# Performance work log

Measured on AMD Instinct MI355X. Metric: run time of the kernel, lower is better.

## Reference

```python
import jax, jax.numpy as jnp
import numpy as np

HIDDEN = 2048
N_HEADS = 32
N_KV = 8
HEAD_DIM = 128
EPS = 1e-6
THETA = 10000.0
WINDOW = 512
T = 2048


def _rms_norm(x, w, eps=EPS):
    # x: [..., d]
    var = jnp.mean(x * x, axis=-1, keepdims=True)
    return x * jax.lax.rsqrt(var + eps) * w


def _rope(x, positions):
    # neox-style full rotary, x: [T, H, d]
    d = x.shape[-1]
    inv_freq = 1.0 / (THETA ** (jnp.arange(0, d, 2, dtype=jnp.float32) / d))  # [d/2]
    ang = positions.astype(jnp.float32)[:, None] * inv_freq  # [T, d/2]
    cos = jnp.cos(ang)[:, None, :]  # [T,1,d/2]
    sin = jnp.sin(ang)[:, None, :]
    x1, x2 = x[..., : d // 2], x[..., d // 2 :]
    return jnp.concatenate([x1 * cos - x2 * sin, x2 * cos + x1 * sin], axis=-1)


def setup_inputs() -> dict:
    key = jax.random.key(0)
    ks = jax.random.split(key, 6)
    q_size = N_HEADS * HEAD_DIM
    kv_size = N_KV * HEAD_DIM
    s = 1.0 / np.sqrt(HIDDEN)
    return {
        "positions": jnp.arange(T, dtype=jnp.int32),
        "hidden_states": jax.random.normal(ks[0], (T, HIDDEN), dtype=jnp.float32),
        "w_qkv": jax.random.normal(ks[1], (HIDDEN, q_size + 2 * kv_size), dtype=jnp.float32) * s,
        "w_o": jax.random.normal(ks[2], (q_size, HIDDEN), dtype=jnp.float32) * s,
        "w_g": jax.random.normal(ks[3], (HIDDEN, N_HEADS), dtype=jnp.float32) * s,
        "q_norm_w": jnp.ones((HEAD_DIM,), dtype=jnp.float32),
        "k_norm_w": jnp.ones((HEAD_DIM,), dtype=jnp.float32),
    }


def reference(positions, hidden_states, w_qkv, w_o, w_g, q_norm_w, k_norm_w):
    t = hidden_states.shape[0]
    q_size = N_HEADS * HEAD_DIM
    kv_size = N_KV * HEAD_DIM
    scale = HEAD_DIM ** -0.5
    group = N_HEADS // N_KV

    qkv = hidden_states @ w_qkv  # [T, q+2kv]
    q = qkv[:, :q_size].reshape(t, N_HEADS, HEAD_DIM)
    k = qkv[:, q_size : q_size + kv_size].reshape(t, N_KV, HEAD_DIM)
    v = qkv[:, q_size + kv_size :].reshape(t, N_KV, HEAD_DIM)

    # per-head RMSNorm then RoPE
    q = _rope(_rms_norm(q, q_norm_w), positions)
    k = _rope(_rms_norm(k, k_norm_w), positions)

    # sliding-window causal attention with GQA (group queries per kv head)
    qg = q.reshape(t, N_KV, group, HEAD_DIM)
    scores = jnp.einsum("tkgd,skd->kgts", qg, k) * scale  # [Hkv,G,T,T]
    diff = positions[:, None] - positions[None, :]  # i - j
    mask = (diff >= 0) & (diff < WINDOW)  # causal + sliding window
    scores = jnp.where(mask[None, None], scores, -jnp.inf)
    probs = jax.nn.softmax(scores, axis=-1)
    attn = jnp.einsum("kgts,skd->tkgd", probs, v).reshape(t, N_HEADS, HEAD_DIM)

    # softplus gate per head, then output projection
    gate = jax.nn.softplus((hidden_states @ w_g).astype(jnp.float32)).astype(attn.dtype)
    attn = attn * gate[:, :, None]
    return attn.reshape(t, q_size) @ w_o
```

## Files before the change

### kernel.cpp

```cpp
#include <hip/hip_runtime.h>

typedef __attribute__((ext_vector_type(4))) float floatx4;
typedef __attribute__((ext_vector_type(8))) _Float16 half8;
typedef __attribute__((ext_vector_type(4))) _Float16 half4;

#define TT 2048
#define HIDDEN 2048
#define NH 32
#define NKV 8
#define HD 128
#define QSIZE 4096
#define KVSIZE 1024
#define QKVN 6144
#define QKVNP 6272
#define WQR 6400
#define VOFF 5120
#define GOFF 6144
#define WINDOW 512

__global__ __launch_bounds__(256) void prep_kernel(
    const float* __restrict__ w_qkv, const float* __restrict__ w_o,
    const float* __restrict__ hidden, const float* __restrict__ w_g,
    _Float16* __restrict__ Wqkvt, _Float16* __restrict__ Wot,
    _Float16* __restrict__ Xb) {
  __shared__ float tile[64][68];
  int bid = blockIdx.x;
  int tid = threadIdx.x;
  if (bid >= 5120) {
    if (bid < 7168) {
      int i = ((bid - 5120) * 256 + tid) * 8;
      float4 a = *(const float4*)&hidden[i];
      float4 b = *(const float4*)&hidden[i + 4];
      alignas(16) _Float16 o[8] = {(_Float16)a.x, (_Float16)a.y, (_Float16)a.z, (_Float16)a.w,
                                   (_Float16)b.x, (_Float16)b.y, (_Float16)b.z, (_Float16)b.w};
      *(uint4*)&Xb[i] = *(const uint4*)o;
    } else if (bid < 7392) {
      int i = ((bid - 7168) * 256 + tid) * 8;
      *(uint4*)&Wqkvt[(size_t)(GOFF + NH) * HIDDEN + i] = (uint4){0, 0, 0, 0};
    } else {
      int br = (bid - 7392) * 32;
      int c = tid & 31, r0 = tid >> 5;
      __shared__ float gt[32][33];
#pragma unroll
      for (int i = 0; i < 4; ++i) {
        int r = r0 + 8 * i;
        gt[r][c] = w_g[(size_t)(br + r) * NH + c];
      }
      __syncthreads();
#pragma unroll
      for (int i = 0; i < 4; ++i) {
        int r = r0 + 8 * i;
        Wqkvt[(size_t)(GOFF + r) * HIDDEN + br + c] = (_Float16)gt[c][r];
      }
    }
    return;
  }
  const float* in;
  _Float16* out;
  int R, C, tilesX, t;
  if (bid < 3072) { in = w_qkv; out = Wqkvt; R = HIDDEN; C = QKVN; tilesX = 96; t = bid; }
  else           { in = w_o;   out = Wot;   R = QSIZE;  C = HIDDEN; tilesX = 32; t = bid - 3072; }
  int bc = (t % tilesX) * 64, br = (t / tilesX) * 64;
  int rr = tid >> 4, l16 = tid & 15;
#pragma unroll
  for (int it = 0; it < 4; ++it) {
    int r = rr + it * 16;
    *(float4*)&tile[r][l16 * 4] = *(const float4*)&in[(size_t)(br + r) * C + bc + l16 * 4];
  }
  __syncthreads();
  int orow = tid >> 2, rr0 = (tid & 3) * 16;
  alignas(16) _Float16 tmp[16];
#pragma unroll
  for (int jj = 0; jj < 16; ++jj) tmp[jj] = (_Float16)tile[rr0 + jj][orow];
  *(uint4*)&out[(size_t)(bc + orow) * R + br + rr0] = *(const uint4*)&tmp[0];
  *(uint4*)&out[(size_t)(bc + orow) * R + br + rr0 + 8] = *(const uint4*)&tmp[8];
}

__global__ __launch_bounds__(256) void repack_v_kernel(const _Float16* __restrict__ QKVh,
                                                       _Float16* __restrict__ Vf) {
  __shared__ _Float16 tile[64][136];
  int st = blockIdx.x, kh = blockIdx.y;
  int s0 = st * 64;
#pragma unroll
  for (int i = 0; i < 4; ++i) {
    int c = threadIdx.x + i * 256;
    int row = c >> 4, part = c & 15;
    *(uint4*)&tile[row][part * 8] =
        *(const uint4*)&QKVh[(size_t)(s0 + row) * QKVNP + VOFF + kh * HD + part * 8];
  }
  __syncthreads();
  _Float16* dst = Vf + (size_t)(kh * 32 + st) * 8192;
#pragma unroll
  for (int i = 0; i < 4; ++i) {
    int c = threadIdx.x + i * 256;
    int jd = c >> 7, kc = (c >> 6) & 1, quad = (c >> 4) & 3, n16 = c & 15;
    int d = jd * 16 + n16, sb = kc * 32 + quad * 8;
    alignas(16) _Float16 tmp[8];
#pragma unroll
    for (int j = 0; j < 8; ++j) tmp[j] = tile[sb + j][d];
    *(uint4*)&dst[c * 8] = *(const uint4*)tmp;
  }
}

__device__ __forceinline__ void async16(const _Float16* g, _Float16* l) {
  __builtin_amdgcn_global_load_lds((const __attribute__((address_space(1))) void*)g,
                                   (__attribute__((address_space(3))) void*)l, 16, 0, 0);
}

#define G256_K 2048

#define STG_A(ob, mh, kt)                                                        \
  async16(As0 + (size_t)(mh) * 64 * G256_K + (kt), &lds[(ob) + ((mh) * 64 + r0A0) * 64]); \
  async16(As1 + (size_t)(mh) * 64 * G256_K + (kt), &lds[(ob) + ((mh) * 64 + r0A1) * 64]);
#define STG_B(ob, nh, kt)                                                        \
  async16(Bs0 + (size_t)(nh) * 32 * G256_K + (kt), &lds[(ob) + 16384 + ((nh) * 32 + r0B0) * 64]); \
  async16(Bs1 + (size_t)(nh) * 32 * G256_K + (kt), &lds[(ob) + 16384 + ((nh) * 32 + r0B1) * 64]);

#define LD_A(DST, mh)                                                            \
  _Pragma("unroll") for (int fm = 0; fm < 4; ++fm)                               \
  _Pragma("unroll") for (int ks = 0; ks < 2; ++ks)                               \
    DST[fm][ks] = *(const half8*)&LA[(wm * 128 + (mh) * 64 + fm * 16 + lr) * 64 + \
                                     (((ks * 4 + quad) ^ l7) * 8)];
#define LD_B(DST, nh)                                                            \
  _Pragma("unroll") for (int fn = 0; fn < 2; ++fn)                               \
  _Pragma("unroll") for (int ks = 0; ks < 2; ++ks)                               \
    DST[fn][ks] = *(const half8*)&LB[(wn * 64 + (nh) * 32 + fn * 16 + lr) * 64 + \
                                     (((ks * 4 + quad) ^ l7) * 8)];
#define MFMAQ(AS, BS, mh, nh)                                                    \
  __builtin_amdgcn_s_setprio(1);                                                 \
  _Pragma("unroll") for (int fm = 0; fm < 4; ++fm)                               \
  _Pragma("unroll") for (int fn = 0; fn < 2; ++fn)                               \
  _Pragma("unroll") for (int ks = 0; ks < 2; ++ks)                               \
    acc[(mh) * 4 + fm][(nh) * 2 + fn] = __builtin_amdgcn_mfma_f32_16x16x32_f16(  \
        AS[fm][ks], BS[fn][ks], acc[(mh) * 4 + fm][(nh) * 2 + fn], 0, 0, 0);     \
  __builtin_amdgcn_s_setprio(0);
#define VMW0 asm volatile("s_waitcnt vmcnt(0)" ::: "memory")
#define BAR __builtin_amdgcn_s_barrier()
#define SB0 __builtin_amdgcn_sched_barrier(0)

__global__ __launch_bounds__(512, 2) void gemm256_kernel(
    const _Float16* __restrict__ A, const _Float16* __restrict__ Bt,
    _Float16* __restrict__ C) {
  __shared__ _Float16 lds[65536];
  int tid = threadIdx.x;
  int wave = tid >> 6, lane = tid & 63;
  int wm = wave >> 2, wn = wave & 3;
  int lr = lane & 15, quad = lane >> 4, l7 = lane & 7, l3 = lane >> 3;
  int m0 = blockIdx.x * 256, n0 = blockIdx.y * 256;

  int q0 = wave * 2, q1 = q0 + 1;
  int r0A0 = (q0 >> 3) * 128 + (q0 & 7) * 8;
  int r0A1 = (q1 >> 3) * 128 + (q1 & 7) * 8;
  int r0B0 = (q0 >> 2) * 64 + (q0 & 3) * 8;
  int r0B1 = (q1 >> 2) * 64 + (q1 & 3) * 8;
  int gA8 = (l7 ^ l3) * 8;

  const _Float16* As0 = A + (size_t)(m0 + r0A0 + l3) * G256_K + gA8;
  const _Float16* As1 = A + (size_t)(m0 + r0A1 + l3) * G256_K + gA8;
  const _Float16* Bs0 = Bt + (size_t)(n0 + r0B0 + l3) * G256_K + gA8;
  const _Float16* Bs1 = Bt + (size_t)(n0 + r0B1 + l3) * G256_K + gA8;

  floatx4 acc[8][4];
#pragma unroll
  for (int i = 0; i < 8; ++i)
#pragma unroll
    for (int j = 0; j < 4; ++j) acc[i][j] = (floatx4){0.f, 0.f, 0.f, 0.f};

  STG_A(0, 0, 0);
  STG_A(0, 1, 0);
  STG_B(0, 0, 0);
  STG_B(0, 1, 0);
  VMW0;
  BAR;
  SB0;

  half8 a0f[4][2], a1f[4][2], b0[2][2], b1[2][2];

  for (int t = 0; t < 32; ++t) {
    int bb = (t & 1) << 15;
    int ob = bb ^ 32768;
    int ktn = (t + 1) * 64;
    bool stg = (t < 31);
    const _Float16* LA = &lds[bb];
    const _Float16* LB = &lds[bb + 16384];

    if (stg) {
      STG_A(ob, 0, ktn);
      STG_B(ob, 0, ktn);
      STG_B(ob, 1, ktn);
      STG_A(ob, 1, ktn);
    }

    LD_B(b0, 0);
    LD_A(a0f, 0);
    MFMAQ(a0f, b0, 0, 0);
    LD_B(b1, 1);
    MFMAQ(a0f, b1, 0, 1);
    LD_A(a1f, 1);
    MFMAQ(a1f, b0, 1, 0);
    MFMAQ(a1f, b1, 1, 1);

    if (stg) VMW0;
    BAR;
    SB0;
  }

#pragma unroll
  for (int mh = 0; mh < 2; ++mh)
#pragma unroll
    for (int fm = 0; fm < 4; ++fm)
#pragma unroll
      for (int nh = 0; nh < 2; ++nh)
#pragma unroll
        for (int fn = 0; fn < 2; ++fn)
#pragma unroll
          for (int rr = 0; rr < 4; ++rr) {
            int row = m0 + wm * 128 + mh * 64 + fm * 16 + quad * 4 + rr;
            int col = n0 + wn * 64 + nh * 32 + fn * 16 + lr;
            if (col < QKVNP)
              C[(size_t)row * QKVNP + col] = (_Float16)acc[mh * 4 + fm][nh * 2 + fn][rr];
          }
}

__device__ __forceinline__ void swizzle_mn(int& m0, int& n0) {
  int ntiles = gridDim.y;
  int pid = blockIdx.x + blockIdx.y * gridDim.x;
  int band = pid / (8 * ntiles);
  int wi = pid - band * (8 * ntiles);
  m0 = (band * 8 + (wi & 7)) * 128;
  n0 = (wi >> 3) * 128;
}

__global__ __launch_bounds__(256, 2) void gemm_bt_splitk_kernel(
    const _Float16* __restrict__ A, const _Float16* __restrict__ Bt,
    float* __restrict__ Cp, int M, int N, int K, int Ks) {
  __shared__ _Float16 As[128 * 64];
  __shared__ _Float16 Bs[128 * 64];
  int tid = threadIdx.x;
  int wave = tid >> 6, lane = tid & 63;
  int wm = wave >> 1, wn = wave & 1;
  int m0, n0;
  swizzle_mn(m0, n0);
  int kb = blockIdx.z * Ks;
  float* C = Cp + (size_t)blockIdx.z * M * N;
  int lr = lane & 15;
  int quad = lane >> 4;
  floatx4 acc[4][4];
#pragma unroll
  for (int i = 0; i < 4; ++i)
#pragma unroll
    for (int j = 0; j < 4; ++j) acc[i][j] = (floatx4){0.f, 0.f, 0.f, 0.f};

  for (int k0 = kb; k0 < kb + Ks; k0 += 64) {
    __syncthreads();
#pragma unroll
    for (int it = 0; it < 4; ++it) {
      int c = tid + it * 256;
      int row = c >> 3, j = c & 7;
      int jj = j ^ (row & 7);
      _Float16* la = &As[it * 2048 + wave * 512];
      _Float16* lb = &Bs[it * 2048 + wave * 512];
      async16(&A[(size_t)(m0 + row) * K + k0 + jj * 8], la);
      async16(&Bt[(size_t)(n0 + row) * K + k0 + jj * 8], lb);
    }
    __syncthreads();
#pragma unroll
    for (int kc = 0; kc < 2; ++kc) {
      int ch = kc * 4 + quad;
      half8 a[4], b[4];
#pragma unroll
      for (int i = 0; i < 4; ++i) {
        int r = wm * 64 + i * 16 + lr;
        a[i] = *(const half8*)&As[r * 64 + (ch ^ (r & 7)) * 8];
      }
#pragma unroll
      for (int j = 0; j < 4; ++j) {
        int r = wn * 64 + j * 16 + lr;
        b[j] = *(const half8*)&Bs[r * 64 + (ch ^ (r & 7)) * 8];
      }
#pragma unroll
      for (int i = 0; i < 4; ++i)
#pragma unroll
        for (int j = 0; j < 4; ++j)
          acc[i][j] = __builtin_amdgcn_mfma_f32_16x16x32_f16(a[i], b[j], acc[i][j], 0, 0, 0);
    }
  }
  int rq = quad * 4;
#pragma unroll
  for (int i = 0; i < 4; ++i)
#pragma unroll
    for (int j = 0; j < 4; ++j)
#pragma unroll
      for (int r = 0; r < 4; ++r) {
        int row = m0 + wm * 64 + i * 16 + rq + r;
        int col = n0 + wn * 64 + j * 16 + lr;
        C[(size_t)row * N + col] = acc[i][j][r];
      }
}

__global__ __launch_bounds__(256) void reduce2_kernel(const float* __restrict__ P,
                                                      float* __restrict__ out) {
  size_t i = ((size_t)blockIdx.x * 256 + threadIdx.x) * 8;
  const float* Q = P + (size_t)TT * HIDDEN;
  float4 a0 = *(const float4*)&P[i];
  float4 a1 = *(const float4*)&P[i + 4];
  float4 b0 = *(const float4*)&Q[i];
  float4 b1 = *(const float4*)&Q[i + 4];
  a0.x += b0.x; a0.y += b0.y; a0.z += b0.z; a0.w += b0.w;
  a1.x += b1.x; a1.y += b1.y; a1.z += b1.z; a1.w += b1.w;
  *(float4*)&out[i] = a0;
  *(float4*)&out[i + 4] = a1;
}

__global__ __launch_bounds__(256) void normrope_kernel(
    const _Float16* __restrict__ qkv, const float* __restrict__ qw,
    const float* __restrict__ kw, const int* __restrict__ positions,
    _Float16* __restrict__ qh, _Float16* __restrict__ Kf) {
  int wid = blockIdx.x * 4 + (threadIdx.x >> 6);
  int lane = threadIdx.x & 63;
  int t, hh;
  const _Float16* src;
  const float* w;
  bool isq = wid < TT * NH;
  if (isq) {
    t = wid >> 5; hh = wid & 31;
    src = qkv + (size_t)t * QKVNP + hh * HD;
    w = qw;
  } else {
    int r = wid - TT * NH;
    t = r >> 3; hh = r & 7;
    src = qkv + (size_t)t * QKVNP + QSIZE + hh * HD;
    w = kw;
  }
  float x1 = (float)src[lane];
  float x2 = (float)src[lane + 64];
  float ss = x1 * x1 + x2 * x2;
#pragma unroll
  for (int off = 1; off < 64; off <<= 1) ss += __shfl_xor(ss, off);
  float rr = rsqrtf(ss * (1.0f / 128.0f) + 1e-6f);
  float n1 = x1 * rr * w[lane];
  float n2 = x2 * rr * w[lane + 64];
  float pos = (float)positions[t];
  float invf = exp2f(-(float)lane * (13.287712379549449f / 64.0f));
  float ang = pos * invf;
  float sn, cs;
  sincosf(ang, &sn, &cs);
  float r1 = n1 * cs - n2 * sn;
  float r2 = n2 * cs + n1 * sn;
  if (isq) {
    _Float16* dst = qh + ((size_t)t * NH + hh) * HD;
    dst[lane] = (_Float16)r1;
    dst[lane + 64] = (_Float16)r2;
  } else {
    int st = t >> 6, jt = (t >> 4) & 3, n16 = t & 15;
    _Float16* kb = Kf + (size_t)(hh * 32 + st) * 8192;
    int c = jt * 256 + (lane >> 5) * 64 + ((lane >> 3) & 3) * 16 + n16;
    kb[c * 8 + (lane & 7)] = (_Float16)r1;
    kb[(c + 128) * 8 + (lane & 7)] = (_Float16)r2;
  }
}

#define PSTR 68
#define M0 8.0f
__global__ __launch_bounds__(256, 2) void attn_kernel(
    const _Float16* __restrict__ Qh, const _Float16* __restrict__ Kf,
    const _Float16* __restrict__ Vf, const _Float16* __restrict__ QKVh,
    _Float16* __restrict__ Og) {
  const float scale = 0.08838834764831845f;
  __shared__ _Float16 Ps[4][16 * PSTR];
  int tid = threadIdx.x;
  int wave = tid >> 6, lane = tid & 63;
  int n16 = lane & 15, quad = lane >> 4;
  int t0 = blockIdx.x * 16;
  int kh = blockIdx.y;
  int h = kh * 4 + wave;
  _Float16* ps = Ps[wave];

  half8 qf[4];
#pragma unroll
  for (int kc = 0; kc < 4; ++kc)
    qf[kc] = *(const half8*)&Qh[((size_t)(t0 + n16) * NH + h) * HD + kc * 32 + quad * 8];

  floatx4 O[8];
  float lp[4];
#pragma unroll
  for (int jd = 0; jd < 8; ++jd) O[jd] = (floatx4){0.f, 0.f, 0.f, 0.f};
#pragma unroll
  for (int r = 0; r < 4; ++r) lp[r] = 0.f;

  int lo = t0 - (WINDOW - 1);
  if (lo < 0) lo = 0;
  int st0 = lo >> 6;
  int st1 = t0 >> 6;

  half8 kfr[4][4];
  {
    const _Float16* kb = Kf + (size_t)(kh * 32 + st0) * 8192;
#pragma unroll
    for (int jt = 0; jt < 4; ++jt)
#pragma unroll
      for (int kc = 0; kc < 4; ++kc)
        kfr[jt][kc] = *(const half8*)&kb[(jt * 4 + kc) * 512 + lane * 8];
  }

  for (int st = st0; st <= st1; ++st) {
    int s0 = st * 64;
    const _Float16* vb = Vf + (size_t)(kh * 32 + st) * 8192;
    floatx4 S[4];
#pragma unroll
    for (int jt = 0; jt < 4; ++jt) S[jt] = (floatx4){0.f, 0.f, 0.f, 0.f};
#pragma unroll
    for (int jt = 0; jt < 4; ++jt)
#pragma unroll
      for (int kc = 0; kc < 4; ++kc)
        S[jt] = __builtin_amdgcn_mfma_f32_16x16x32_f16(qf[kc], kfr[jt][kc], S[jt], 0, 0, 0);
    if (st < st1) {
      const _Float16* kb = Kf + (size_t)(kh * 32 + st + 1) * 8192;
#pragma unroll
      for (int jt = 0; jt < 4; ++jt)
#pragma unroll
        for (int kc = 0; kc < 4; ++kc)
          kfr[jt][kc] = *(const half8*)&kb[(jt * 4 + kc) * 512 + lane * 8];
    }
    bool interior = (t0 >= s0 + 63) && (t0 + 15 - s0 < WINDOW);
    if (interior) {
#pragma unroll
      for (int r = 0; r < 4; ++r) {
        float rs = 0.f;
#pragma unroll
        for (int jt = 0; jt < 4; ++jt) {
          float p = __expf(__builtin_fmaf(S[jt][r], scale, -M0));
          rs += p;
          ps[(quad * 4 + r) * PSTR + jt * 16 + n16] = (_Float16)p;
        }
        lp[r] += rs;
      }
    } else {
#pragma unroll
      for (int r = 0; r < 4; ++r) {
        int tq = t0 + quad * 4 + r;
        float rs = 0.f;
#pragma unroll
        for (int jt = 0; jt < 4; ++jt) {
          int diff = tq - (s0 + jt * 16 + n16);
          bool ok = (diff >= 0) && (diff < WINDOW);
          float p = ok ? __expf(__builtin_fmaf(S[jt][r], scale, -M0)) : 0.f;
          rs += p;
          ps[(quad * 4 + r) * PSTR + jt * 16 + n16] = (_Float16)p;
        }
        lp[r] += rs;
      }
    }
    half8 pf[2];
#pragma unroll
    for (int kc = 0; kc < 2; ++kc) {
      half4 lo4 = *(const half4*)&ps[n16 * PSTR + kc * 32 + quad * 8];
      half4 hi4 = *(const half4*)&ps[n16 * PSTR + kc * 32 + quad * 8 + 4];
      pf[kc] = (half8){lo4[0], lo4[1], lo4[2], lo4[3], hi4[0], hi4[1], hi4[2], hi4[3]};
    }
#pragma unroll
    for (int jd = 0; jd < 8; ++jd) {
#pragma unroll
      for (int kc = 0; kc < 2; ++kc) {
        half8 vfr = *(const half8*)&vb[(jd * 2 + kc) * 512 + lane * 8];
        O[jd] = __builtin_amdgcn_mfma_f32_16x16x32_f16(pf[kc], vfr, O[jd], 0, 0, 0);
      }
    }
  }
#pragma unroll
  for (int r = 0; r < 4; ++r) {
    float l = lp[r];
#pragma unroll
    for (int off = 1; off < 16; off <<= 1) l += __shfl_xor(l, off);
    int t = t0 + quad * 4 + r;
    float gl = (float)QKVh[(size_t)t * QKVNP + GOFF + h];
    float g = (gl > 0.f) ? gl + log1pf(__expf(-gl)) : log1pf(__expf(gl));
    float inv = g / l;
#pragma unroll
    for (int jd = 0; jd < 8; ++jd)
      Og[(size_t)t * QSIZE + h * HD + jd * 16 + n16] = (_Float16)(O[jd][r] * inv);
  }
}

extern "C" void kernel_launch(void* const* d_in, const int* in_sizes, int n_in,
                              void* d_out, int out_size, void* d_ws, size_t ws_size,
                              hipStream_t stream) {
  const int* positions = (const int*)d_in[0];
  const float* hidden = (const float*)d_in[1];
  const float* w_qkv = (const float*)d_in[2];
  const float* w_o = (const float*)d_in[3];
  const float* w_g = (const float*)d_in[4];
  const float* q_norm_w = (const float*)d_in[5];
  const float* k_norm_w = (const float*)d_in[6];
  float* out = (float*)d_out;

  char* ws = (char*)d_ws;
  size_t off = 0;
  auto alloc = [&](size_t bytes) {
    void* p = ws + off;
    off += (bytes + 255) & ~(size_t)255;
    return p;
  };
  _Float16* Xb = (_Float16*)alloc((size_t)TT * HIDDEN * 2);
  _Float16* Wqkvt = (_Float16*)alloc((size_t)WQR * HIDDEN * 2);
  _Float16* Wot = (_Float16*)alloc((size_t)HIDDEN * QSIZE * 2);
  _Float16* QKVh = (_Float16*)alloc((size_t)TT * QKVNP * 2);
  _Float16* Qh = (_Float16*)alloc((size_t)TT * NH * HD * 2);
  _Float16* Kf = (_Float16*)alloc((size_t)NKV * 32 * 8192 * 2);
  _Float16* Vf = (_Float16*)alloc((size_t)NKV * 32 * 8192 * 2);
  _Float16* Og = (_Float16*)alloc((size_t)TT * QSIZE * 2);
  float* Cp = (float*)ws;

  prep_kernel<<<7456, 256, 0, stream>>>(w_qkv, w_o, hidden, w_g, Wqkvt, Wot, Xb);
  gemm256_kernel<<<dim3(TT / 256, WQR / 256), 512, 0, stream>>>(Xb, Wqkvt, QKVh);
  normrope_kernel<<<(TT * (NH + NKV)) / 4, 256, 0, stream>>>(QKVh, q_norm_w, k_norm_w,
                                                             positions, Qh, Kf);
  repack_v_kernel<<<dim3(32, NKV), 256, 0, stream>>>(QKVh, Vf);
  attn_kernel<<<dim3(TT / 16, NKV), 256, 0, stream>>>(Qh, Kf, Vf, QKVh, Og);
  gemm_bt_splitk_kernel<<<dim3(TT / 128, HIDDEN / 128, 2), 256, 0, stream>>>(
      Og, Wot, Cp, TT, HIDDEN, QSIZE, QSIZE / 2);
  reduce2_kernel<<<(TT * HIDDEN) / (256 * 8), 256, 0, stream>>>(Cp, out);
}
```

Before: 314.7 us.

## Fuse RMSNorm, RoPE, K/V repacking and gate extraction into the QKV GEMM epilogue

Each QKV GEMM tile epilogue now applies per-head RMSNorm and RoPE and writes Q and K directly in the layouts attention expects. It also scatters V into the attention-ready packed layout and writes the gate logits to a compact buffer. The prep kernel gains a precomputed cos/sin table. This removes the QKVh intermediate and the separate normrope and repack_v kernels, saving global round trips and launches. The cost is a heavier epilogue with LDS exchanges between paired waves, extra barriers and scattered 2-byte stores.

```diff
diff --git a/kernel.cpp b/kernel.cpp
--- a/kernel.cpp
+++ b/kernel.cpp
@@ -12,17 +12,16 @@
 #define QSIZE 4096
 #define KVSIZE 1024
 #define QKVN 6144
-#define QKVNP 6272
 #define WQR 6400
-#define VOFF 5120
 #define GOFF 6144
 #define WINDOW 512
 
 __global__ __launch_bounds__(256) void prep_kernel(
     const float* __restrict__ w_qkv, const float* __restrict__ w_o,
     const float* __restrict__ hidden, const float* __restrict__ w_g,
+    const int* __restrict__ positions,
     _Float16* __restrict__ Wqkvt, _Float16* __restrict__ Wot,
-    _Float16* __restrict__ Xb) {
+    _Float16* __restrict__ Xb, float* __restrict__ tbl) {
   __shared__ float tile[64][68];
   int bid = blockIdx.x;
   int tid = threadIdx.x;
@@ -37,7 +36,7 @@
     } else if (bid < 7392) {
       int i = ((bid - 7168) * 256 + tid) * 8;
       *(uint4*)&Wqkvt[(size_t)(GOFF + NH) * HIDDEN + i] = (uint4){0, 0, 0, 0};
-    } else {
+    } else if (bid < 7456) {
       int br = (bid - 7392) * 32;
       int c = tid & 31, r0 = tid >> 5;
       __shared__ float gt[32][33];
@@ -52,6 +51,15 @@
         int r = r0 + 8 * i;
         Wqkvt[(size_t)(GOFF + r) * HIDDEN + br + c] = (_Float16)gt[c][r];
       }
+    } else {
+      int idx = (bid - 7456) * 256 + tid;
+      int t = idx >> 6, j = idx & 63;
+      float pos = (float)positions[t];
+      float invf = exp2f(-(float)j * (13.287712379549449f / 64.0f));
+      float sn, cs;
+      sincosf(pos * invf, &sn, &cs);
+      tbl[t * 128 + j] = cs;
+      tbl[t * 128 + 64 + j] = sn;
     }
     return;
   }
@@ -74,32 +82,6 @@
   for (int jj = 0; jj < 16; ++jj) tmp[jj] = (_Float16)tile[rr0 + jj][orow];
   *(uint4*)&out[(size_t)(bc + orow) * R + br + rr0] = *(const uint4*)&tmp[0];
   *(uint4*)&out[(size_t)(bc + orow) * R + br + rr0 + 8] = *(const uint4*)&tmp[8];
-}
-
-__global__ __launch_bounds__(256) void repack_v_kernel(const _Float16* __restrict__ QKVh,
-                                                       _Float16* __restrict__ Vf) {
-  __shared__ _Float16 tile[64][136];
-  int st = blockIdx.x, kh = blockIdx.y;
-  int s0 = st * 64;
-#pragma unroll
-  for (int i = 0; i < 4; ++i) {
-    int c = threadIdx.x + i * 256;
-    int row = c >> 4, part = c & 15;
-    *(uint4*)&tile[row][part * 8] =
-        *(const uint4*)&QKVh[(size_t)(s0 + row) * QKVNP + VOFF + kh * HD + part * 8];
-  }
-  __syncthreads();
-  _Float16* dst = Vf + (size_t)(kh * 32 + st) * 8192;
-#pragma unroll
-  for (int i = 0; i < 4; ++i) {
-    int c = threadIdx.x + i * 256;
-    int jd = c >> 7, kc = (c >> 6) & 1, quad = (c >> 4) & 3, n16 = c & 15;
-    int d = jd * 16 + n16, sb = kc * 32 + quad * 8;
-    alignas(16) _Float16 tmp[8];
-#pragma unroll
-    for (int j = 0; j < 8; ++j) tmp[j] = tile[sb + j][d];
-    *(uint4*)&dst[c * 8] = *(const uint4*)tmp;
-  }
 }
 
 __device__ __forceinline__ void async16(const _Float16* g, _Float16* l) {
@@ -140,7 +122,10 @@
 
 __global__ __launch_bounds__(512, 2) void gemm256_kernel(
     const _Float16* __restrict__ A, const _Float16* __restrict__ Bt,
-    _Float16* __restrict__ C) {
+    const float* __restrict__ tbl, const float* __restrict__ qw,
+    const float* __restrict__ kw, _Float16* __restrict__ Qh,
+    _Float16* __restrict__ Kf, _Float16* __restrict__ Vf,
+    _Float16* __restrict__ Gate) {
   __shared__ _Float16 lds[65536];
   int tid = threadIdx.x;
   int wave = tid >> 6, lane = tid & 63;
@@ -205,21 +190,137 @@
     SB0;
   }
 
-#pragma unroll
-  for (int mh = 0; mh < 2; ++mh)
-#pragma unroll
-    for (int fm = 0; fm < 4; ++fm)
-#pragma unroll
-      for (int nh = 0; nh < 2; ++nh)
-#pragma unroll
-        for (int fn = 0; fn < 2; ++fn)
-#pragma unroll
-          for (int rr = 0; rr < 4; ++rr) {
-            int row = m0 + wm * 128 + mh * 64 + fm * 16 + quad * 4 + rr;
-            int col = n0 + wn * 64 + nh * 32 + fn * 16 + lr;
-            if (col < QKVNP)
-              C[(size_t)row * QKVNP + col] = (_Float16)acc[mh * 4 + fm][nh * 2 + fn][rr];
-          }
+  int nt = blockIdx.y;
+  int wn1 = wn & 1;
+  int hloc = wn >> 1;
+
+  if (nt < 20) {
+    const float* w = (nt < 16) ? qw : kw;
+    float wlo[2][2], whi[2][2];
+#pragma unroll
+    for (int nh = 0; nh < 2; ++nh)
+#pragma unroll
+      for (int fn = 0; fn < 2; ++fn) {
+        int c0 = nh * 32 + fn * 16 + lr;
+        wlo[nh][fn] = w[c0];
+        whi[nh][fn] = w[c0 + 64];
+      }
+    _Float16* ldh = lds;
+    float* lsum = (float*)&lds[8 * 64 * 68];
+#pragma unroll
+    for (int mh = 0; mh < 2; ++mh) {
+      float s[4][4];
+#pragma unroll
+      for (int fm = 0; fm < 4; ++fm)
+#pragma unroll
+        for (int rq = 0; rq < 4; ++rq) {
+          float sv = 0.f;
+#pragma unroll
+          for (int nh = 0; nh < 2; ++nh)
+#pragma unroll
+            for (int fn = 0; fn < 2; ++fn) {
+              float v = acc[mh * 4 + fm][nh * 2 + fn][rq];
+              sv += v * v;
+            }
+#pragma unroll
+          for (int off = 1; off < 16; off <<= 1) sv += __shfl_xor(sv, off);
+          s[fm][rq] = sv;
+        }
+#pragma unroll
+      for (int fm = 0; fm < 4; ++fm)
+#pragma unroll
+        for (int nh = 0; nh < 2; ++nh)
+#pragma unroll
+          for (int fn = 0; fn < 2; ++fn)
+#pragma unroll
+            for (int rq = 0; rq < 4; ++rq) {
+              int row = fm * 16 + quad * 4 + rq;
+              ldh[(wave * 64 + row) * 68 + nh * 32 + fn * 16 + lr] =
+                  (_Float16)acc[mh * 4 + fm][nh * 2 + fn][rq];
+            }
+      if (lr == 0) {
+#pragma unroll
+        for (int fm = 0; fm < 4; ++fm)
+#pragma unroll
+          for (int rq = 0; rq < 4; ++rq)
+            lsum[wave * 64 + fm * 16 + quad * 4 + rq] = s[fm][rq];
+      }
+      __syncthreads();
+      int pw = wave ^ 1;
+#pragma unroll
+      for (int fm = 0; fm < 4; ++fm)
+#pragma unroll
+        for (int rq = 0; rq < 4; ++rq) {
+          int row = fm * 16 + quad * 4 + rq;
+          int t = m0 + wm * 128 + mh * 64 + row;
+          float inv = rsqrtf((s[fm][rq] + lsum[pw * 64 + row]) * 0.0078125f + 1e-6f);
+          const float* tb = &tbl[(size_t)t * 128];
+#pragma unroll
+          for (int nh = 0; nh < 2; ++nh)
+#pragma unroll
+            for (int fn = 0; fn < 2; ++fn) {
+              int c0 = nh * 32 + fn * 16 + lr;
+              float xo = acc[mh * 4 + fm][nh * 2 + fn][rq];
+              float xp = (float)ldh[(pw * 64 + row) * 68 + c0];
+              float cs = tb[c0], sn = tb[64 + c0];
+              float out;
+              if (wn1 == 0)
+                out = (xo * inv * wlo[nh][fn]) * cs - (xp * inv * whi[nh][fn]) * sn;
+              else
+                out = (xo * inv * whi[nh][fn]) * cs + (xp * inv * wlo[nh][fn]) * sn;
+              if (nt < 16) {
+                int h = nt * 2 + hloc;
+                int d = wn1 * 64 + c0;
+                Qh[((size_t)t * NH + h) * HD + d] = (_Float16)out;
+              } else {
+                int kh = (nt - 16) * 2 + hloc;
+                _Float16* kb = Kf + ((size_t)kh * 32 + (t >> 6)) * 8192;
+                int jt = (t >> 4) & 3, n16 = t & 15;
+                int c = jt * 256 + (c0 >> 5) * 64 + ((c0 >> 3) & 3) * 16 + n16;
+                kb[(c + wn1 * 128) * 8 + (c0 & 7)] = (_Float16)out;
+              }
+            }
+        }
+      __syncthreads();
+    }
+  } else if (nt < 24) {
+#pragma unroll
+    for (int mh = 0; mh < 2; ++mh)
+#pragma unroll
+      for (int fm = 0; fm < 4; ++fm)
+#pragma unroll
+        for (int nh = 0; nh < 2; ++nh)
+#pragma unroll
+          for (int fn = 0; fn < 2; ++fn)
+#pragma unroll
+            for (int rq = 0; rq < 4; ++rq) {
+              int row = fm * 16 + quad * 4 + rq;
+              int t = m0 + wm * 128 + mh * 64 + row;
+              int cg = wn * 64 + nh * 32 + fn * 16 + lr;
+              int kh = (nt - 20) * 2 + (cg >> 7);
+              int d = cg & 127;
+              int sv = t & 63;
+              _Float16* vb = Vf + ((size_t)kh * 32 + (t >> 6)) * 8192;
+              int c = (d >> 4) * 128 + (sv >> 5) * 64 + ((sv >> 3) & 3) * 16 + (d & 15);
+              vb[c * 8 + (sv & 7)] = (_Float16)acc[mh * 4 + fm][nh * 2 + fn][rq];
+            }
+  } else {
+    if (wn == 0) {
+#pragma unroll
+      for (int mh = 0; mh < 2; ++mh)
+#pragma unroll
+        for (int fm = 0; fm < 4; ++fm)
+#pragma unroll
+          for (int fn = 0; fn < 2; ++fn)
+#pragma unroll
+            for (int rq = 0; rq < 4; ++rq) {
+              int row = fm * 16 + quad * 4 + rq;
+              int t = m0 + wm * 128 + mh * 64 + row;
+              int col = fn * 16 + lr;
+              Gate[(size_t)t * NH + col] = (_Float16)acc[mh * 4 + fm][fn][rq];
+            }
+    }
+  }
 }
 
 __device__ __forceinline__ void swizzle_mn(int& m0, int& n0) {
@@ -312,59 +413,11 @@
   *(float4*)&out[i + 4] = a1;
 }
 
-__global__ __launch_bounds__(256) void normrope_kernel(
-    const _Float16* __restrict__ qkv, const float* __restrict__ qw,
-    const float* __restrict__ kw, const int* __restrict__ positions,
-    _Float16* __restrict__ qh, _Float16* __restrict__ Kf) {
-  int wid = blockIdx.x * 4 + (threadIdx.x >> 6);
-  int lane = threadIdx.x & 63;
-  int t, hh;
-  const _Float16* src;
-  const float* w;
-  bool isq = wid < TT * NH;
-  if (isq) {
-    t = wid >> 5; hh = wid & 31;
-    src = qkv + (size_t)t * QKVNP + hh * HD;
-    w = qw;
-  } else {
-    int r = wid - TT * NH;
-    t = r >> 3; hh = r & 7;
-    src = qkv + (size_t)t * QKVNP + QSIZE + hh * HD;
-    w = kw;
-  }
-  float x1 = (float)src[lane];
-  float x2 = (float)src[lane + 64];
-  float ss = x1 * x1 + x2 * x2;
-#pragma unroll
-  for (int off = 1; off < 64; off <<= 1) ss += __shfl_xor(ss, off);
-  float rr = rsqrtf(ss * (1.0f / 128.0f) + 1e-6f);
-  float n1 = x1 * rr * w[lane];
-  float n2 = x2 * rr * w[lane + 64];
-  float pos = (float)positions[t];
-  float invf = exp2f(-(float)lane * (13.287712379549449f / 64.0f));
-  float ang = pos * invf;
-  float sn, cs;
-  sincosf(ang, &sn, &cs);
-  float r1 = n1 * cs - n2 * sn;
-  float r2 = n2 * cs + n1 * sn;
-  if (isq) {
-    _Float16* dst = qh + ((size_t)t * NH + hh) * HD;
-    dst[lane] = (_Float16)r1;
-    dst[lane + 64] = (_Float16)r2;
-  } else {
-    int st = t >> 6, jt = (t >> 4) & 3, n16 = t & 15;
-    _Float16* kb = Kf + (size_t)(hh * 32 + st) * 8192;
-    int c = jt * 256 + (lane >> 5) * 64 + ((lane >> 3) & 3) * 16 + n16;
-    kb[c * 8 + (lane & 7)] = (_Float16)r1;
-    kb[(c + 128) * 8 + (lane & 7)] = (_Float16)r2;
-  }
-}
-
 #define PSTR 68
 #define M0 8.0f
 __global__ __launch_bounds__(256, 2) void attn_kernel(
     const _Float16* __restrict__ Qh, const _Float16* __restrict__ Kf,
-    const _Float16* __restrict__ Vf, const _Float16* __restrict__ QKVh,
+    const _Float16* __restrict__ Vf, const _Float16* __restrict__ Gate,
     _Float16* __restrict__ Og) {
   const float scale = 0.08838834764831845f;
   __shared__ _Float16 Ps[4][16 * PSTR];
@@ -473,7 +526,7 @@
 #pragma unroll
     for (int off = 1; off < 16; off <<= 1) l += __shfl_xor(l, off);
     int t = t0 + quad * 4 + r;
-    float gl = (float)QKVh[(size_t)t * QKVNP + GOFF + h];
+    float gl = (float)Gate[(size_t)t * NH + h];
     float g = (gl > 0.f) ? gl + log1pf(__expf(-gl)) : log1pf(__expf(gl));
     float inv = g / l;
 #pragma unroll
@@ -504,19 +557,19 @@
   _Float16* Xb = (_Float16*)alloc((size_t)TT * HIDDEN * 2);
   _Float16* Wqkvt = (_Float16*)alloc((size_t)WQR * HIDDEN * 2);
   _Float16* Wot = (_Float16*)alloc((size_t)HIDDEN * QSIZE * 2);
-  _Float16* QKVh = (_Float16*)alloc((size_t)TT * QKVNP * 2);
   _Float16* Qh = (_Float16*)alloc((size_t)TT * NH * HD * 2);
   _Float16* Kf = (_Float16*)alloc((size_t)NKV * 32 * 8192 * 2);
   _Float16* Vf = (_Float16*)alloc((size_t)NKV * 32 * 8192 * 2);
   _Float16* Og = (_Float16*)alloc((size_t)TT * QSIZE * 2);
+  _Float16* Gate = (_Float16*)alloc((size_t)TT * NH * 2);
+  float* CosSin = (float*)alloc((size_t)TT * 128 * 4);
   float* Cp = (float*)ws;
 
-  prep_kernel<<<7456, 256, 0, stream>>>(w_qkv, w_o, hidden, w_g, Wqkvt, Wot, Xb);
-  gemm256_kernel<<<dim3(TT / 256, WQR / 256), 512, 0, stream>>>(Xb, Wqkvt, QKVh);
-  normrope_kernel<<<(TT * (NH + NKV)) / 4, 256, 0, stream>>>(QKVh, q_norm_w, k_norm_w,
-                                                             positions, Qh, Kf);
-  repack_v_kernel<<<dim3(32, NKV), 256, 0, stream>>>(QKVh, Vf);
-  attn_kernel<<<dim3(TT / 16, NKV), 256, 0, stream>>>(Qh, Kf, Vf, QKVh, Og);
+  prep_kernel<<<7968, 256, 0, stream>>>(w_qkv, w_o, hidden, w_g, positions,
+                                        Wqkvt, Wot, Xb, CosSin);
+  gemm256_kernel<<<dim3(TT / 256, WQR / 256), 512, 0, stream>>>(
+      Xb, Wqkvt, CosSin, q_norm_w, k_norm_w, Qh, Kf, Vf, Gate);
+  attn_kernel<<<dim3(TT / 16, NKV), 256, 0, stream>>>(Qh, Kf, Vf, Gate, Og);
   gemm_bt_splitk_kernel<<<dim3(TT / 128, HIDDEN / 128, 2), 256, 0, stream>>>(
       Og, Wot, Cp, TT, HIDDEN, QSIZE, QSIZE / 2);
   reduce2_kernel<<<(TT * HIDDEN) / (256 * 8), 256, 0, stream>>>(Cp, out);
```

Measured after the change: 317.9 us. No clear change (+1.0%).

## Fuse V repack and gate split into QKV GEMM epilogue; precompute RoPE table

Applied to the files above, without the earlier changes.

The QKV GEMM epilogue now writes Q/K to a narrower buffer, scatters V straight into the attention-friendly fragment layout, and writes the gate logits to a compact buffer. This removes the separate repack_v kernel and one round trip of V through global memory. RoPE cos/sin values are computed once per position in the prep kernel and read from a table, so normrope no longer evaluates sincos for every head. The trade-off is that the V epilogue does scattered 2-byte stores with poor coalescing.

```diff
diff --git a/kernel.cpp b/kernel.cpp
--- a/kernel.cpp
+++ b/kernel.cpp
@@ -12,17 +12,17 @@
 #define QSIZE 4096
 #define KVSIZE 1024
 #define QKVN 6144
-#define QKVNP 6272
 #define WQR 6400
-#define VOFF 5120
 #define GOFF 6144
+#define QKSTR 5120
 #define WINDOW 512
 
 __global__ __launch_bounds__(256) void prep_kernel(
     const float* __restrict__ w_qkv, const float* __restrict__ w_o,
     const float* __restrict__ hidden, const float* __restrict__ w_g,
+    const int* __restrict__ positions,
     _Float16* __restrict__ Wqkvt, _Float16* __restrict__ Wot,
-    _Float16* __restrict__ Xb) {
+    _Float16* __restrict__ Xb, float* __restrict__ tbl) {
   __shared__ float tile[64][68];
   int bid = blockIdx.x;
   int tid = threadIdx.x;
@@ -37,7 +37,7 @@
     } else if (bid < 7392) {
       int i = ((bid - 7168) * 256 + tid) * 8;
       *(uint4*)&Wqkvt[(size_t)(GOFF + NH) * HIDDEN + i] = (uint4){0, 0, 0, 0};
-    } else {
+    } else if (bid < 7456) {
       int br = (bid - 7392) * 32;
       int c = tid & 31, r0 = tid >> 5;
       __shared__ float gt[32][33];
@@ -52,6 +52,15 @@
         int r = r0 + 8 * i;
         Wqkvt[(size_t)(GOFF + r) * HIDDEN + br + c] = (_Float16)gt[c][r];
       }
+    } else {
+      int idx = (bid - 7456) * 256 + tid;
+      int t = idx >> 6, j = idx & 63;
+      float pos = (float)positions[t];
+      float invf = exp2f(-(float)j * (13.287712379549449f / 64.0f));
+      float sn, cs;
+      sincosf(pos * invf, &sn, &cs);
+      tbl[t * 128 + j] = cs;
+      tbl[t * 128 + 64 + j] = sn;
     }
     return;
   }
@@ -74,32 +83,6 @@
   for (int jj = 0; jj < 16; ++jj) tmp[jj] = (_Float16)tile[rr0 + jj][orow];
   *(uint4*)&out[(size_t)(bc + orow) * R + br + rr0] = *(const uint4*)&tmp[0];
   *(uint4*)&out[(size_t)(bc + orow) * R + br + rr0 + 8] = *(const uint4*)&tmp[8];
-}
-
-__global__ __launch_bounds__(256) void repack_v_kernel(const _Float16* __restrict__ QKVh,
-                                                       _Float16* __restrict__ Vf) {
-  __shared__ _Float16 tile[64][136];
-  int st = blockIdx.x, kh = blockIdx.y;
-  int s0 = st * 64;
-#pragma unroll
-  for (int i = 0; i < 4; ++i) {
-    int c = threadIdx.x + i * 256;
-    int row = c >> 4, part = c & 15;
-    *(uint4*)&tile[row][part * 8] =
-        *(const uint4*)&QKVh[(size_t)(s0 + row) * QKVNP + VOFF + kh * HD + part * 8];
-  }
-  __syncthreads();
-  _Float16* dst = Vf + (size_t)(kh * 32 + st) * 8192;
-#pragma unroll
-  for (int i = 0; i < 4; ++i) {
-    int c = threadIdx.x + i * 256;
-    int jd = c >> 7, kc = (c >> 6) & 1, quad = (c >> 4) & 3, n16 = c & 15;
-    int d = jd * 16 + n16, sb = kc * 32 + quad * 8;
-    alignas(16) _Float16 tmp[8];
-#pragma unroll
-    for (int j = 0; j < 8; ++j) tmp[j] = tile[sb + j][d];
-    *(uint4*)&dst[c * 8] = *(const uint4*)tmp;
-  }
 }
 
 __device__ __forceinline__ void async16(const _Float16* g, _Float16* l) {
@@ -140,7 +123,8 @@
 
 __global__ __launch_bounds__(512, 2) void gemm256_kernel(
     const _Float16* __restrict__ A, const _Float16* __restrict__ Bt,
-    _Float16* __restrict__ C) {
+    _Float16* __restrict__ QKb, _Float16* __restrict__ Vf,
+    _Float16* __restrict__ Gate) {
   __shared__ _Float16 lds[65536];
   int tid = threadIdx.x;
   int wave = tid >> 6, lane = tid & 63;
@@ -205,21 +189,105 @@
     SB0;
   }
 
-#pragma unroll
-  for (int mh = 0; mh < 2; ++mh)
-#pragma unroll
-    for (int fm = 0; fm < 4; ++fm)
-#pragma unroll
-      for (int nh = 0; nh < 2; ++nh)
-#pragma unroll
-        for (int fn = 0; fn < 2; ++fn)
-#pragma unroll
-          for (int rr = 0; rr < 4; ++rr) {
-            int row = m0 + wm * 128 + mh * 64 + fm * 16 + quad * 4 + rr;
-            int col = n0 + wn * 64 + nh * 32 + fn * 16 + lr;
-            if (col < QKVNP)
-              C[(size_t)row * QKVNP + col] = (_Float16)acc[mh * 4 + fm][nh * 2 + fn][rr];
-          }
+  int nt = blockIdx.y;
+  if (nt < 20) {
+#pragma unroll
+    for (int mh = 0; mh < 2; ++mh)
+#pragma unroll
+      for (int fm = 0; fm < 4; ++fm)
+#pragma unroll
+        for (int nh = 0; nh < 2; ++nh)
+#pragma unroll
+          for (int fn = 0; fn < 2; ++fn)
+#pragma unroll
+            for (int rr = 0; rr < 4; ++rr) {
+              int row = m0 + wm * 128 + mh * 64 + fm * 16 + quad * 4 + rr;
+              int col = nt * 256 + wn * 64 + nh * 32 + fn * 16 + lr;
+              QKb[(size_t)row * QKSTR + col] = (_Float16)acc[mh * 4 + fm][nh * 2 + fn][rr];
+            }
+  } else if (nt < 24) {
+#pragma unroll
+    for (int mh = 0; mh < 2; ++mh)
+#pragma unroll
+      for (int fm = 0; fm < 4; ++fm)
+#pragma unroll
+        for (int nh = 0; nh < 2; ++nh)
+#pragma unroll
+          for (int fn = 0; fn < 2; ++fn)
+#pragma unroll
+            for (int rq = 0; rq < 4; ++rq) {
+              int row = fm * 16 + quad * 4 + rq;
+              int t = m0 + wm * 128 + mh * 64 + row;
+              int cg = wn * 64 + nh * 32 + fn * 16 + lr;
+              int kh = (nt - 20) * 2 + (cg >> 7);
+              int d = cg & 127;
+              int sv = t & 63;
+              _Float16* vb = Vf + ((size_t)kh * 32 + (t >> 6)) * 8192;
+              int c = (d >> 4) * 128 + (sv >> 5) * 64 + ((sv >> 3) & 3) * 16 + (d & 15);
+              vb[c * 8 + (sv & 7)] = (_Float16)acc[mh * 4 + fm][nh * 2 + fn][rq];
+            }
+  } else {
+    if (wn == 0) {
+#pragma unroll
+      for (int mh = 0; mh < 2; ++mh)
+#pragma unroll
+        for (int fm = 0; fm < 4; ++fm)
+#pragma unroll
+          for (int fn = 0; fn < 2; ++fn)
+#pragma unroll
+            for (int rq = 0; rq < 4; ++rq) {
+              int row = fm * 16 + quad * 4 + rq;
+              int t = m0 + wm * 128 + mh * 64 + row;
+              int col = fn * 16 + lr;
+              Gate[(size_t)t * NH + col] = (_Float16)acc[mh * 4 + fm][fn][rq];
+            }
+    }
+  }
+}
+
+__global__ __launch_bounds__(256) void normrope_kernel(
+    const _Float16* __restrict__ QKb, const float* __restrict__ qw,
+    const float* __restrict__ kw, const float* __restrict__ tbl,
+    _Float16* __restrict__ qh, _Float16* __restrict__ Kf) {
+  int wid = blockIdx.x * 4 + (threadIdx.x >> 6);
+  int lane = threadIdx.x & 63;
+  int t, hh;
+  const _Float16* src;
+  const float* w;
+  bool isq = wid < TT * NH;
+  if (isq) {
+    t = wid >> 5; hh = wid & 31;
+    src = QKb + (size_t)t * QKSTR + hh * HD;
+    w = qw;
+  } else {
+    int r = wid - TT * NH;
+    t = r >> 3; hh = r & 7;
+    src = QKb + (size_t)t * QKSTR + QSIZE + hh * HD;
+    w = kw;
+  }
+  float x1 = (float)src[lane];
+  float x2 = (float)src[lane + 64];
+  float ss = x1 * x1 + x2 * x2;
+#pragma unroll
+  for (int off = 1; off < 64; off <<= 1) ss += __shfl_xor(ss, off);
+  float rr = rsqrtf(ss * (1.0f / 128.0f) + 1e-6f);
+  float n1 = x1 * rr * w[lane];
+  float n2 = x2 * rr * w[lane + 64];
+  float cs = tbl[(size_t)t * 128 + lane];
+  float sn = tbl[(size_t)t * 128 + 64 + lane];
+  float r1 = n1 * cs - n2 * sn;
+  float r2 = n2 * cs + n1 * sn;
+  if (isq) {
+    _Float16* dst = qh + ((size_t)t * NH + hh) * HD;
+    dst[lane] = (_Float16)r1;
+    dst[lane + 64] = (_Float16)r2;
+  } else {
+    int st = t >> 6, jt = (t >> 4) & 3, n16 = t & 15;
+    _Float16* kb = Kf + (size_t)(hh * 32 + st) * 8192;
+    int c = jt * 256 + (lane >> 5) * 64 + ((lane >> 3) & 3) * 16 + n16;
+    kb[c * 8 + (lane & 7)] = (_Float16)r1;
+    kb[(c + 128) * 8 + (lane & 7)] = (_Float16)r2;
+  }
 }
 
 __device__ __forceinline__ void swizzle_mn(int& m0, int& n0) {
@@ -312,59 +380,11 @@
   *(float4*)&out[i + 4] = a1;
 }
 
-__global__ __launch_bounds__(256) void normrope_kernel(
-    const _Float16* __restrict__ qkv, const float* __restrict__ qw,
-    const float* __restrict__ kw, const int* __restrict__ positions,
-    _Float16* __restrict__ qh, _Float16* __restrict__ Kf) {
-  int wid = blockIdx.x * 4 + (threadIdx.x >> 6);
-  int lane = threadIdx.x & 63;
-  int t, hh;
-  const _Float16* src;
-  const float* w;
-  bool isq = wid < TT * NH;
-  if (isq) {
-    t = wid >> 5; hh = wid & 31;
-    src = qkv + (size_t)t * QKVNP + hh * HD;
-    w = qw;
-  } else {
-    int r = wid - TT * NH;
-    t = r >> 3; hh = r & 7;
-    src = qkv + (size_t)t * QKVNP + QSIZE + hh * HD;
-    w = kw;
-  }
-  float x1 = (float)src[lane];
-  float x2 = (float)src[lane + 64];
-  float ss = x1 * x1 + x2 * x2;
-#pragma unroll
-  for (int off = 1; off < 64; off <<= 1) ss += __shfl_xor(ss, off);
-  float rr = rsqrtf(ss * (1.0f / 128.0f) + 1e-6f);
-  float n1 = x1 * rr * w[lane];
-  float n2 = x2 * rr * w[lane + 64];
-  float pos = (float)positions[t];
-  float invf = exp2f(-(float)lane * (13.287712379549449f / 64.0f));
-  float ang = pos * invf;
-  float sn, cs;
-  sincosf(ang, &sn, &cs);
-  float r1 = n1 * cs - n2 * sn;
-  float r2 = n2 * cs + n1 * sn;
-  if (isq) {
-    _Float16* dst = qh + ((size_t)t * NH + hh) * HD;
-    dst[lane] = (_Float16)r1;
-    dst[lane + 64] = (_Float16)r2;
-  } else {
-    int st = t >> 6, jt = (t >> 4) & 3, n16 = t & 15;
-    _Float16* kb = Kf + (size_t)(hh * 32 + st) * 8192;
-    int c = jt * 256 + (lane >> 5) * 64 + ((lane >> 3) & 3) * 16 + n16;
-    kb[c * 8 + (lane & 7)] = (_Float16)r1;
-    kb[(c + 128) * 8 + (lane & 7)] = (_Float16)r2;
-  }
-}
-
 #define PSTR 68
 #define M0 8.0f
 __global__ __launch_bounds__(256, 2) void attn_kernel(
     const _Float16* __restrict__ Qh, const _Float16* __restrict__ Kf,
-    const _Float16* __restrict__ Vf, const _Float16* __restrict__ QKVh,
+    const _Float16* __restrict__ Vf, const _Float16* __restrict__ Gate,
     _Float16* __restrict__ Og) {
   const float scale = 0.08838834764831845f;
   __shared__ _Float16 Ps[4][16 * PSTR];
@@ -473,7 +493,7 @@
 #pragma unroll
     for (int off = 1; off < 16; off <<= 1) l += __shfl_xor(l, off);
     int t = t0 + quad * 4 + r;
-    float gl = (float)QKVh[(size_t)t * QKVNP + GOFF + h];
+    float gl = (float)Gate[(size_t)t * NH + h];
     float g = (gl > 0.f) ? gl + log1pf(__expf(-gl)) : log1pf(__expf(gl));
     float inv = g / l;
 #pragma unroll
@@ -504,19 +524,22 @@
   _Float16* Xb = (_Float16*)alloc((size_t)TT * HIDDEN * 2);
   _Float16* Wqkvt = (_Float16*)alloc((size_t)WQR * HIDDEN * 2);
   _Float16* Wot = (_Float16*)alloc((size_t)HIDDEN * QSIZE * 2);
-  _Float16* QKVh = (_Float16*)alloc((size_t)TT * QKVNP * 2);
+  _Float16* QKb = (_Float16*)alloc((size_t)TT * QKSTR * 2);
   _Float16* Qh = (_Float16*)alloc((size_t)TT * NH * HD * 2);
   _Float16* Kf = (_Float16*)alloc((size_t)NKV * 32 * 8192 * 2);
   _Float16* Vf = (_Float16*)alloc((size_t)NKV * 32 * 8192 * 2);
   _Float16* Og = (_Float16*)alloc((size_t)TT * QSIZE * 2);
+  _Float16* Gate = (_Float16*)alloc((size_t)TT * NH * 2);
+  float* CosSin = (float*)alloc((size_t)TT * 128 * 4);
   float* Cp = (float*)ws;
 
-  prep_kernel<<<7456, 256, 0, stream>>>(w_qkv, w_o, hidden, w_g, Wqkvt, Wot, Xb);
-  gemm256_kernel<<<dim3(TT / 256, WQR / 256), 512, 0, stream>>>(Xb, Wqkvt, QKVh);
-  normrope_kernel<<<(TT * (NH + NKV)) / 4, 256, 0, stream>>>(QKVh, q_norm_w, k_norm_w,
-                                                             positions, Qh, Kf);
-  repack_v_kernel<<<dim3(32, NKV), 256, 0, stream>>>(QKVh, Vf);
-  attn_kernel<<<dim3(TT / 16, NKV), 256, 0, stream>>>(Qh, Kf, Vf, QKVh, Og);
+  prep_kernel<<<7968, 256, 0, stream>>>(w_qkv, w_o, hidden, w_g, positions,
+                                        Wqkvt, Wot, Xb, CosSin);
+  gemm256_kernel<<<dim3(TT / 256, WQR / 256), 512, 0, stream>>>(
+      Xb, Wqkvt, QKb, Vf, Gate);
+  normrope_kernel<<<(TT * (NH + NKV)) / 4, 256, 0, stream>>>(QKb, q_norm_w, k_norm_w,
+                                                             CosSin, Qh, Kf);
+  attn_kernel<<<dim3(TT / 16, NKV), 256, 0, stream>>>(Qh, Kf, Vf, Gate, Og);
   gemm_bt_splitk_kernel<<<dim3(TT / 128, HIDDEN / 128, 2), 256, 0, stream>>>(
       Og, Wot, Cp, TT, HIDDEN, QSIZE, QSIZE / 2);
   reduce2_kernel<<<(TT * HIDDEN) / (256 * 8), 256, 0, stream>>>(Cp, out);
```

Result: no change. 320.9 us (+2.0%).
